# Performance work log

Measured on AMD Instinct MI355X. Metric: run time of the kernel, lower is better.

Reference implementation:

```python
import jax, jax.numpy as jnp
import numpy as np

NUM_NODES = 50000
NUM_HYPEREDGES = 50000
NNZ = 800000
IN_CH, HID_CH, OUT_CH = 512, 256, 64


def setup_inputs() -> dict:
    key = jax.random.key(0)
    k = jax.random.split(key, 6)
    x = jax.random.normal(k[0], (NUM_NODES, IN_CH), dtype=jnp.float32)
    node_idx = jax.random.randint(k[1], (NNZ,), 0, NUM_NODES)
    hedge_idx = jax.random.randint(k[2], (NNZ,), 0, NUM_HYPEREDGES)
    edge_index = jnp.stack([node_idx, hedge_idx]).astype(jnp.int64)
    W1 = jax.random.normal(k[3], (IN_CH, HID_CH), dtype=jnp.float32) * (1.0 / np.sqrt(IN_CH))
    b1 = jnp.zeros((HID_CH,), dtype=jnp.float32)
    W2 = jax.random.normal(k[4], (HID_CH, OUT_CH), dtype=jnp.float32) * (1.0 / np.sqrt(HID_CH))
    b2 = jnp.zeros((OUT_CH,), dtype=jnp.float32)
    return {"x": x, "edge_index": edge_index, "W1": W1, "b1": b1, "W2": W2, "b2": b2}


def hypergraph_conv(x, node_idx, hedge_idx, W, b):
    # x' = D^{-1} H B^{-1} H^T (x Theta) + b   (PyG HypergraphConv, unit edge weights)
    h = x @ W                                   # [N, F_out]
    ones = jnp.ones(node_idx.shape[0], dtype=x.dtype)
    D = jax.ops.segment_sum(ones, node_idx, num_segments=NUM_NODES)        # node degree
    B = jax.ops.segment_sum(ones, hedge_idx, num_segments=NUM_HYPEREDGES)  # hyperedge degree
    D_inv = jnp.where(D > 0, 1.0 / D, 0.0)
    B_inv = jnp.where(B > 0, 1.0 / B, 0.0)
    # node -> hyperedge aggregation
    m = jax.ops.segment_sum(h[node_idx], hedge_idx, num_segments=NUM_HYPEREDGES)
    m = m * B_inv[:, None]                      # [E, F_out]
    # hyperedge -> node aggregation
    out = jax.ops.segment_sum(m[hedge_idx], node_idx, num_segments=NUM_NODES)
    out = out * D_inv[:, None]                  # [N, F_out]
    return out + b


def reference(x, edge_index, W1, b1, W2, b2):
    node_idx = edge_index[0]
    hedge_idx = edge_index[1]
    h = hypergraph_conv(x, node_idx, hedge_idx, W1, b1)
    h = jax.nn.relu(h)
    h = hypergraph_conv(h, node_idx, hedge_idx, W2, b2)
    return jax.nn.log_softmax(h, axis=1)
```

## Files before the change

kernel.cpp:

```cpp
#include <hip/hip_runtime.h>
#include <math.h>

#define N_NODES  50000
#define N_HEDGES 50000
#define NNZ_     800000
#define IN_CH    512
#define HID_CH   256
#define OUT_CH   64
#define M_PAD    50048
#define NBK      391

#define BH_BLK   98
#define PK1_BLK  512
#define PK2_BLK  64

typedef __attribute__((ext_vector_type(8))) short bf16x8;
typedef __attribute__((ext_vector_type(4))) float f32x4;

__device__ __forceinline__ unsigned short f2bf(float f) {
    union { float f; unsigned u; } v; v.f = f;
    unsigned r = v.u + 0x7FFFu + ((v.u >> 16) & 1u);
    return (unsigned short)(r >> 16);
}
__device__ __forceinline__ float bf2f(unsigned short u) {
    union { unsigned u; float f; } v; v.u = (unsigned)u << 16; return v.f;
}

#define GLL16(g, l)                                                            \
    __builtin_amdgcn_global_load_lds(                                          \
        (const __attribute__((address_space(1))) void*)(g),                    \
        (__attribute__((address_space(3))) void*)(l), 16, 0, 0)

__global__ void prep_kernel(const float* __restrict__ W1, unsigned short* __restrict__ Wp1,
                            const float* __restrict__ W2, unsigned short* __restrict__ Wp2,
                            const int* __restrict__ ni, const int* __restrict__ hi,
                            int* __restrict__ bcntN, int* __restrict__ bcntH) {
    const int blk = blockIdx.x;
    const int t = threadIdx.x;
    if (blk < BH_BLK) {
        __shared__ int lh[NBK], ln[NBK];
        for (int k = t; k < NBK; k += 256) { lh[k] = 0; ln[k] = 0; }
        __syncthreads();
        for (int i4 = blk * 256 + t; i4 < NNZ_ / 4; i4 += BH_BLK * 256) {
            const int4 nv = *(const int4*)(ni + i4 * 4);
            const int4 hv = *(const int4*)(hi + i4 * 4);
            atomicAdd(&ln[nv.x >> 7], 1); atomicAdd(&ln[nv.y >> 7], 1);
            atomicAdd(&ln[nv.z >> 7], 1); atomicAdd(&ln[nv.w >> 7], 1);
            atomicAdd(&lh[hv.x >> 7], 1); atomicAdd(&lh[hv.y >> 7], 1);
            atomicAdd(&lh[hv.z >> 7], 1); atomicAdd(&lh[hv.w >> 7], 1);
        }
        __syncthreads();
        for (int k = t; k < NBK; k += 256) {
            if (ln[k]) atomicAdd(&bcntN[k], ln[k]);
            if (lh[k]) atomicAdd(&bcntH[k], lh[k]);
        }
    } else if (blk < BH_BLK + PK1_BLK) {
        const int i = (blk - BH_BLK) * 256 + t;
        const int kt = i / (HID_CH * 32);
        const int r  = i % (HID_CH * 32);
        const int n  = r >> 5, kk = r & 31;
        Wp1[i] = f2bf(W1[(size_t)(kt * 32 + kk) * HID_CH + n]);
    } else {
        const int i = (blk - (BH_BLK + PK1_BLK)) * 256 + t;
        const int kt = i / (OUT_CH * 32);
        const int r  = i % (OUT_CH * 32);
        const int n  = r >> 5, kk = r & 31;
        Wp2[i] = f2bf(W2[(size_t)(kt * 32 + kk) * OUT_CH + n]);
    }
}

__global__ void scan391_kernel(const int* __restrict__ cA, int* __restrict__ offA,
                               int* __restrict__ curA,
                               const int* __restrict__ cB, int* __restrict__ offB,
                               int* __restrict__ curB) {
    const int* cnt = blockIdx.x ? cB : cA;
    int* off = blockIdx.x ? offB : offA;
    int* cur = blockIdx.x ? curB : curA;
    __shared__ int sbuf[512];
    const int t = threadIdx.x;
    const int v = (t < NBK) ? cnt[t] : 0;
    sbuf[t] = v;
    __syncthreads();
    #pragma unroll
    for (int d = 1; d < 512; d <<= 1) {
        int u = (t >= d) ? sbuf[t - d] : 0;
        __syncthreads();
        sbuf[t] += u;
        __syncthreads();
    }
    if (t < NBK) { off[t] = sbuf[t] - v; cur[t] = sbuf[t] - v; }
    if (t == NBK - 1) off[NBK] = sbuf[t];
}

__global__ void bin_kernel(const int* __restrict__ ni, const int* __restrict__ hi,
                           int* __restrict__ bcurN, int* __restrict__ bcurH,
                           unsigned* __restrict__ recN, unsigned* __restrict__ recH) {
    __shared__ int cH[NBK], cN[NBK], bH[NBK], bN[NBK];
    for (int t = threadIdx.x; t < NBK; t += blockDim.x) { cH[t] = 0; cN[t] = 0; }
    __syncthreads();
    const int gid = blockIdx.x * blockDim.x + threadIdx.x;
    const int i0 = gid * 4;
    int4 nv, hv;
    const bool act = (i0 < NNZ_);
    if (act) {
        nv = *(const int4*)(ni + i0);
        hv = *(const int4*)(hi + i0);
        atomicAdd(&cN[nv.x >> 7], 1); atomicAdd(&cN[nv.y >> 7], 1);
        atomicAdd(&cN[nv.z >> 7], 1); atomicAdd(&cN[nv.w >> 7], 1);
        atomicAdd(&cH[hv.x >> 7], 1); atomicAdd(&cH[hv.y >> 7], 1);
        atomicAdd(&cH[hv.z >> 7], 1); atomicAdd(&cH[hv.w >> 7], 1);
    }
    __syncthreads();
    for (int t = threadIdx.x; t < NBK; t += blockDim.x) {
        bH[t] = cH[t] ? atomicAdd(&bcurH[t], cH[t]) : 0;
        bN[t] = cN[t] ? atomicAdd(&bcurN[t], cN[t]) : 0;
    }
    __syncthreads();
    for (int t = threadIdx.x; t < NBK; t += blockDim.x) { cH[t] = bH[t]; cN[t] = bN[t]; }
    __syncthreads();
    if (act) {
        int nn[4] = {nv.x, nv.y, nv.z, nv.w};
        int hh[4] = {hv.x, hv.y, hv.z, hv.w};
        #pragma unroll
        for (int k = 0; k < 4; ++k) {
            int p = atomicAdd(&cH[hh[k] >> 7], 1);
            recH[p] = ((unsigned)(hh[k] & 127) << 16) | (unsigned)nn[k];
            p = atomicAdd(&cN[nn[k] >> 7], 1);
            recN[p] = ((unsigned)(nn[k] & 127) << 16) | (unsigned)hh[k];
        }
    }
}

__global__ void buildcsr_kernel(const int* __restrict__ bstartH, const unsigned* __restrict__ recH,
                                int* __restrict__ offH, int* __restrict__ colH,
                                float* __restrict__ Binv,
                                const int* __restrict__ bstartN, const unsigned* __restrict__ recN,
                                int* __restrict__ offN, int* __restrict__ colN,
                                float* __restrict__ Dinv) {
    int b = blockIdx.x;
    const int* bstart; const unsigned* rec; int* off; int* col; float* inv;
    if (b < NBK) { bstart = bstartH; rec = recH; off = offH; col = colH; inv = Binv; }
    else { b -= NBK; bstart = bstartN; rec = recN; off = offN; col = colN; inv = Dinv; }
    const int s = bstart[b], e = bstart[b + 1];
    const int t = threadIdx.x;
    __shared__ int lc[128], ps[128], cur[128];
    if (t < 128) lc[t] = 0;
    __syncthreads();
    for (int i = s + t; i < e; i += 256) atomicAdd(&lc[rec[i] >> 16], 1);
    __syncthreads();
    if (t < 128) ps[t] = lc[t];
    __syncthreads();
    #pragma unroll
    for (int d = 1; d < 128; d <<= 1) {
        int v = (t >= d && t < 128) ? ps[t - d] : 0;
        __syncthreads();
        if (t < 128) ps[t] += v;
        __syncthreads();
    }
    if (t < 128) {
        const int excl = s + ps[t] - lc[t];
        cur[t] = excl;
        const int id = b * 128 + t;
        if (id < N_NODES) {
            off[id] = excl;
            inv[id] = lc[t] > 0 ? 1.f / (float)lc[t] : 0.f;
        }
    }
    if (b == NBK - 1 && t == 255) off[N_NODES] = bstart[NBK];
    __syncthreads();
    for (int i = s + t; i < e; i += 256) {
        const unsigned r = rec[i];
        const int p = atomicAdd(&cur[r >> 16], 1);
        col[p] = (int)(r & 0xFFFFu);
    }
}

__global__ void gemm1_fused_kernel(const float* __restrict__ X,
                                   const unsigned short* __restrict__ Wp,
                                   unsigned short* __restrict__ C, int M) {
    constexpr int BM = 64, BN = 256, K = IN_CH, KT = K / 32;
    __shared__ unsigned short As[BM * 32];
    __shared__ unsigned short Bs[BN * 32];
    const int tid  = threadIdx.x;
    const int wave = tid >> 6;
    const int lane = tid & 63;
    const int wr = wave >> 1;
    const int wc = wave & 1;
    const int quad = lane >> 4;
    const int l15  = lane & 15;
    const int row0 = blockIdx.x * BM;

    float4 va[2];
    auto loadA = [&](int kt) {
        #pragma unroll
        for (int r = 0; r < 2; ++r) {
            const int idx = r * 256 + tid;
            const int row = idx >> 3;
            const int kc  = (idx & 7) * 4;
            const int gr  = row0 + row;
            float4 v = make_float4(0.f, 0.f, 0.f, 0.f);
            if (gr < M) v = *(const float4*)(X + (size_t)gr * K + kt * 32 + kc);
            va[r] = v;
        }
    };

    f32x4 acc[2][8];
    #pragma unroll
    for (int mt = 0; mt < 2; ++mt)
        #pragma unroll
        for (int nt = 0; nt < 8; ++nt)
            acc[mt][nt] = (f32x4)0.f;

    loadA(0);
    for (int kt = 0; kt < KT; ++kt) {
        __syncthreads();
        #pragma unroll
        for (int r = 0; r < 2; ++r) {
            const int idx = r * 256 + tid;
            const int row = idx >> 3;
            const int kc  = (idx & 7) * 4;
            ushort4 o;
            o.x = f2bf(va[r].x); o.y = f2bf(va[r].y);
            o.z = f2bf(va[r].z); o.w = f2bf(va[r].w);
            *(ushort4*)(As + row * 32 + kc) = o;
        }
        const size_t bk = (size_t)kt * BN * 32;
        #pragma unroll
        for (int r = 0; r < 4; ++r)
            GLL16(Wp + bk + r * 2048 + (size_t)tid * 8, Bs + r * 2048 + tid * 8);
        __syncthreads();
        if (kt + 1 < KT) loadA(kt + 1);

        bf16x8 af[2], bfr[8];
        #pragma unroll
        for (int mt = 0; mt < 2; ++mt)
            af[mt] = *(const bf16x8*)(As + (wr * 32 + mt * 16 + l15) * 32 + quad * 8);
        #pragma unroll
        for (int nt = 0; nt < 8; ++nt)
            bfr[nt] = *(const bf16x8*)(Bs + (wc * 128 + nt * 16 + l15) * 32 + quad * 8);
        #pragma unroll
        for (int mt = 0; mt < 2; ++mt)
            #pragma unroll
            for (int nt = 0; nt < 8; ++nt)
                acc[mt][nt] = __builtin_amdgcn_mfma_f32_16x16x32_bf16(
                    af[mt], bfr[nt], acc[mt][nt], 0, 0, 0);
    }

    #pragma unroll
    for (int mt = 0; mt < 2; ++mt) {
        const int gr0 = row0 + wr * 32 + mt * 16 + quad * 4;
        #pragma unroll
        for (int nt = 0; nt < 8; ++nt) {
            const int gc = wc * 128 + nt * 16 + l15;
            #pragma unroll
            for (int r = 0; r < 4; ++r) {
                const int gr = gr0 + r;
                if (gr < M) C[(size_t)gr * HID_CH + gc] = f2bf(acc[mt][nt][r]);
            }
        }
    }
}

template <int BN>
__global__ void mfma_gemm_kernel(const unsigned short* __restrict__ A,
                                 const unsigned short* __restrict__ Wp,
                                 unsigned short* __restrict__ C, int M, int N, int K) {
    constexpr int NT = BN / 32;
    __shared__ unsigned short As[128 * 32];
    __shared__ unsigned short Bs[BN * 32];

    const int tid  = threadIdx.x;
    const int wave = tid >> 6;
    const int lane = tid & 63;
    const int wr = wave >> 1;
    const int wc = wave & 1;
    const int quad = lane >> 4;
    const int l15  = lane & 15;
    const int row0 = blockIdx.y * 128;
    const int col0 = blockIdx.x * BN;

    const size_t a_g0   = (size_t)(row0 + wave * 16 + (lane >> 2)) * K + (lane & 3) * 8;
    const int    a_l0   = (wave * 16 + (lane >> 2)) * 32 + (lane & 3) * 8;
    const size_t b_gbase = ((size_t)col0 + wave * 16 + (lane >> 2)) * 32 + (lane & 3) * 8;
    const int    b_l0   = (wave * 16 + (lane >> 2)) * 32 + (lane & 3) * 8;

    f32x4 acc[4][NT];
    #pragma unroll
    for (int mt = 0; mt < 4; ++mt)
        #pragma unroll
        for (int nt = 0; nt < NT; ++nt)
            acc[mt][nt] = (f32x4)0.f;

    const int KT = K / 32;
    for (int kt = 0; kt < KT; ++kt) {
        __syncthreads();
        GLL16(A + a_g0 + (size_t)kt * 32, As + a_l0);
        GLL16(A + a_g0 + (size_t)(kt * 32) + (size_t)64 * K, As + a_l0 + 64 * 32);
        const size_t bk = (size_t)kt * N * 32;
        GLL16(Wp + bk + b_gbase, Bs + b_l0);
        if (BN == 128)
            GLL16(Wp + bk + b_gbase + 64 * 32, Bs + b_l0 + 64 * 32);
        __syncthreads();

        bf16x8 af[4], bf[NT];
        #pragma unroll
        for (int mt = 0; mt < 4; ++mt)
            af[mt] = *(const bf16x8*)(As + (wr * 64 + mt * 16 + l15) * 32 + quad * 8);
        #pragma unroll
        for (int nt = 0; nt < NT; ++nt)
            bf[nt] = *(const bf16x8*)(Bs + (wc * (BN / 2) + nt * 16 + l15) * 32 + quad * 8);
        #pragma unroll
        for (int mt = 0; mt < 4; ++mt)
            #pragma unroll
            for (int nt = 0; nt < NT; ++nt)
                acc[mt][nt] = __builtin_amdgcn_mfma_f32_16x16x32_bf16(
                    af[mt], bf[nt], acc[mt][nt], 0, 0, 0);
    }

    #pragma unroll
    for (int mt = 0; mt < 4; ++mt) {
        const int gr0 = row0 + wr * 64 + mt * 16 + quad * 4;
        #pragma unroll
        for (int nt = 0; nt < NT; ++nt) {
            const int gc = col0 + wc * (BN / 2) + nt * 16 + l15;
            #pragma unroll
            for (int r = 0; r < 4; ++r) {
                int gr = gr0 + r;
                if (gr < M) C[(size_t)gr * N + gc] = f2bf(acc[mt][nt][r]);
            }
        }
    }
}

template <bool EPI>
__global__ void gather256_kernel(const unsigned short* __restrict__ src,
                                 unsigned short* __restrict__ dst,
                                 const int* __restrict__ off, const int* __restrict__ col,
                                 const float* __restrict__ scale,
                                 const float* __restrict__ bias, int nrows) {
    int row = blockIdx.x * (blockDim.x >> 6) + (threadIdx.x >> 6);
    if (row >= nrows) return;
    const int lane = threadIdx.x & 63;
    const int g = lane >> 5;
    const int l = lane & 31;
    const int s = off[row], e = off[row + 1];
    float a[8];
    #pragma unroll
    for (int k = 0; k < 8; ++k) a[k] = 0.f;
    int j = s + g;
    for (; j + 2 < e; j += 4) {
        const bf16x8 u0 = *(const bf16x8*)(src + ((size_t)col[j]     << 8) + (l << 3));
        const bf16x8 u1 = *(const bf16x8*)(src + ((size_t)col[j + 2] << 8) + (l << 3));
        #pragma unroll
        for (int k = 0; k < 8; ++k)
            a[k] += bf2f((unsigned short)u0[k]) + bf2f((unsigned short)u1[k]);
    }
    if (j < e) {
        const bf16x8 u = *(const bf16x8*)(src + ((size_t)col[j] << 8) + (l << 3));
        #pragma unroll
        for (int k = 0; k < 8; ++k) a[k] += bf2f((unsigned short)u[k]);
    }
    #pragma unroll
    for (int k = 0; k < 8; ++k) a[k] += __shfl_xor(a[k], 32);
    if (g != 0) return;
    const float sc = scale[row];
    float v[8];
    #pragma unroll
    for (int k = 0; k < 8; ++k) v[k] = a[k] * sc;
    if (EPI) {
        const float4 b0 = *(const float4*)(bias + (l << 3));
        const float4 b1 = *(const float4*)(bias + (l << 3) + 4);
        v[0] = fmaxf(v[0] + b0.x, 0.f); v[1] = fmaxf(v[1] + b0.y, 0.f);
        v[2] = fmaxf(v[2] + b0.z, 0.f); v[3] = fmaxf(v[3] + b0.w, 0.f);
        v[4] = fmaxf(v[4] + b1.x, 0.f); v[5] = fmaxf(v[5] + b1.y, 0.f);
        v[6] = fmaxf(v[6] + b1.z, 0.f); v[7] = fmaxf(v[7] + b1.w, 0.f);
    }
    bf16x8 o;
    #pragma unroll
    for (int k = 0; k < 8; ++k) o[k] = (short)f2bf(v[k]);
    *(bf16x8*)(dst + ((size_t)row << 8) + (l << 3)) = o;
}

template <bool LSM>
__global__ void gather64_kernel(const unsigned short* __restrict__ src, void* __restrict__ dstv,
                                const int* __restrict__ off, const int* __restrict__ col,
                                const float* __restrict__ scale,
                                const float* __restrict__ bias, int nrows) {
    int row = blockIdx.x * (blockDim.x >> 6) + (threadIdx.x >> 6);
    if (row >= nrows) return;
    const int lane = threadIdx.x & 63;
    const int g = lane >> 4;
    const int l = lane & 15;
    const int s = off[row], e = off[row + 1];
    float a0 = 0.f, a1 = 0.f, a2 = 0.f, a3 = 0.f;
    int j = s + g;
    for (; j + 4 < e; j += 8) {
        const ushort4 u0 = *(const ushort4*)(src + ((size_t)col[j]     << 6) + (l << 2));
        const ushort4 u1 = *(const ushort4*)(src + ((size_t)col[j + 4] << 6) + (l << 2));
        a0 += bf2f(u0.x) + bf2f(u1.x); a1 += bf2f(u0.y) + bf2f(u1.y);
        a2 += bf2f(u0.z) + bf2f(u1.z); a3 += bf2f(u0.w) + bf2f(u1.w);
    }
    if (j < e) {
        const ushort4 u = *(const ushort4*)(src + ((size_t)col[j] << 6) + (l << 2));
        a0 += bf2f(u.x); a1 += bf2f(u.y); a2 += bf2f(u.z); a3 += bf2f(u.w);
    }
    a0 += __shfl_xor(a0, 16); a1 += __shfl_xor(a1, 16);
    a2 += __shfl_xor(a2, 16); a3 += __shfl_xor(a3, 16);
    a0 += __shfl_xor(a0, 32); a1 += __shfl_xor(a1, 32);
    a2 += __shfl_xor(a2, 32); a3 += __shfl_xor(a3, 32);
    const float sc = scale[row];
    float v0 = a0 * sc, v1 = a1 * sc, v2 = a2 * sc, v3 = a3 * sc;
    if (LSM) {
        const float4 b = *(const float4*)(bias + (l << 2));
        v0 += b.x; v1 += b.y; v2 += b.z; v3 += b.w;
        float m = fmaxf(fmaxf(v0, v1), fmaxf(v2, v3));
        #pragma unroll
        for (int o = 8; o >= 1; o >>= 1) m = fmaxf(m, __shfl_xor(m, o));
        float su = expf(v0 - m) + expf(v1 - m) + expf(v2 - m) + expf(v3 - m);
        #pragma unroll
        for (int o = 8; o >= 1; o >>= 1) su += __shfl_xor(su, o);
        const float lg = m + logf(su);
        if (g == 0) {
            float4 o4;
            o4.x = v0 - lg; o4.y = v1 - lg; o4.z = v2 - lg; o4.w = v3 - lg;
            *(float4*)((float*)dstv + (size_t)row * OUT_CH + (l << 2)) = o4;
        }
    } else if (g == 0) {
        ushort4 o4;
        o4.x = f2bf(v0); o4.y = f2bf(v1); o4.z = f2bf(v2); o4.w = f2bf(v3);
        *(ushort4*)((unsigned short*)dstv + (size_t)row * OUT_CH + (l << 2)) = o4;
    }
}

extern "C" void kernel_launch(void* const* d_in, const int* in_sizes, int n_in,
                              void* d_out, int out_size, void* d_ws, size_t ws_size,
                              hipStream_t stream) {
    const float* x  = (const float*)d_in[0];
    const int*   ei = (const int*)d_in[1];
    const float* W1 = (const float*)d_in[2];
    const float* b1 = (const float*)d_in[3];
    const float* W2 = (const float*)d_in[4];
    const float* b2 = (const float*)d_in[5];
    float* out = (float*)d_out;

    const int* node_idx  = ei;
    const int* hedge_idx = ei + NNZ_;

    const size_t RCAP = (size_t)M_PAD * IN_CH / 2;
    float* regionA = (float*)d_ws;
    float* regionB = regionA + RCAP;
    float* Dinv = regionB + RCAP;
    float* Binv = Dinv + N_NODES;
    int* offN = (int*)(Binv + N_HEDGES);
    int* offH = offN + N_NODES + 1;
    int* colN = offH + N_HEDGES + 1;
    int* colH = colN + NNZ_;
    unsigned short* Wp1 = (unsigned short*)(colH + NNZ_);
    unsigned short* Wp2 = Wp1 + IN_CH * HID_CH;
    int* bcntH   = (int*)(Wp2 + HID_CH * OUT_CH);
    int* bcntN   = bcntH + 400;
    int* bstartH = bcntN + 400;
    int* bstartN = bstartH + 400;
    int* bcurH   = bstartN + 400;
    int* bcurN   = bcurH + 400;

    unsigned* recH = (unsigned*)regionA;
    unsigned* recN = recH + NNZ_;

    unsigned short* h1_bf = (unsigned short*)regionA;
    unsigned short* m1_bf = (unsigned short*)regionB;
    unsigned short* h2_bf = (unsigned short*)regionA;
    unsigned short* g_bf  = (unsigned short*)regionB;
    unsigned short* m2_bf = (unsigned short*)regionB + (size_t)M_PAD * OUT_CH;

    hipMemsetAsync(bcntH, 0, 800 * sizeof(int), stream);
    prep_kernel<<<BH_BLK + PK1_BLK + PK2_BLK, 256, 0, stream>>>(
        W1, Wp1, W2, Wp2, node_idx, hedge_idx, bcntN, bcntH);
    scan391_kernel<<<2, 512, 0, stream>>>(bcntH, bstartH, bcurH, bcntN, bstartN, bcurN);
    bin_kernel<<<200, 1024, 0, stream>>>(node_idx, hedge_idx, bcurN, bcurH, recN, recH);
    buildcsr_kernel<<<2 * NBK, 256, 0, stream>>>(bstartH, recH, offH, colH, Binv,
                                                 bstartN, recN, offN, colN, Dinv);

    gemm1_fused_kernel<<<(N_NODES + 63) / 64, 256, 0, stream>>>(x, Wp1, h1_bf, N_NODES);
    gather256_kernel<false><<<(N_HEDGES + 3) / 4, 256, 0, stream>>>(
        h1_bf, m1_bf, offH, colH, Binv, nullptr, N_HEDGES);
    gather256_kernel<true><<<(N_NODES + 3) / 4, 256, 0, stream>>>(
        m1_bf, h2_bf, offN, colN, Dinv, b1, N_NODES);

    mfma_gemm_kernel<64><<<dim3(OUT_CH / 64, (N_NODES + 127) / 128), 256, 0, stream>>>(
        h2_bf, Wp2, g_bf, N_NODES, OUT_CH, HID_CH);
    gather64_kernel<false><<<(N_HEDGES + 3) / 4, 256, 0, stream>>>(
        g_bf, m2_bf, offH, colH, Binv, nullptr, N_HEDGES);
    gather64_kernel<true><<<(N_NODES + 3) / 4, 256, 0, stream>>>(
        m2_bf, out, offN, colN, Dinv, b2, N_NODES);
}
```

Before: 401.8 us.

## Fuse CSR construction into one cooperative kernel and widen gather64 loads

Replaces the memset plus four preprocessing kernels (count, scan, bin, build CSR) with a single cooperative kernel that uses grid.sync between phases, cutting launch overhead and inter-kernel gaps. The bucket offsets are recomputed per block in shared memory instead of being stored to global memory. Separately, gather64 now has each lane load 8 bf16 values (16 bytes) instead of 4, with 8 neighbour groups per row, and the shuffle reductions are adjusted to match. The cooperative launch relies on 256 blocks of 1024 threads all being resident at once, and grid syncs add their own cost.

```diff
diff --git a/kernel.cpp b/kernel.cpp
--- a/kernel.cpp
+++ b/kernel.cpp
@@ -1,5 +1,8 @@
 #include <hip/hip_runtime.h>
+#include <hip/hip_cooperative_groups.h>
 #include <math.h>
+
+namespace cg = cooperative_groups;
 
 #define N_NODES  50000
 #define N_HEDGES 50000
@@ -10,10 +13,6 @@
 #define M_PAD    50048
 #define NBK      391
 
-#define BH_BLK   98
-#define PK1_BLK  512
-#define PK2_BLK  64
-
 typedef __attribute__((ext_vector_type(8))) short bf16x8;
 typedef __attribute__((ext_vector_type(4))) float f32x4;
 
@@ -31,147 +30,162 @@
         (const __attribute__((address_space(1))) void*)(g),                    \
         (__attribute__((address_space(3))) void*)(l), 16, 0, 0)
 
-__global__ void prep_kernel(const float* __restrict__ W1, unsigned short* __restrict__ Wp1,
-                            const float* __restrict__ W2, unsigned short* __restrict__ Wp2,
-                            const int* __restrict__ ni, const int* __restrict__ hi,
-                            int* __restrict__ bcntN, int* __restrict__ bcntH) {
+#define AST(p, v) __hip_atomic_store((p), (v), __ATOMIC_RELAXED, __HIP_MEMORY_SCOPE_AGENT)
+#define ALD(p)    __hip_atomic_load((p), __ATOMIC_RELAXED, __HIP_MEMORY_SCOPE_AGENT)
+
+__global__ __launch_bounds__(1024, 4) void csr_coop_kernel(
+    const float* __restrict__ W1, unsigned short* __restrict__ Wp1,
+    const float* __restrict__ W2, unsigned short* __restrict__ Wp2,
+    const int* __restrict__ ni, const int* __restrict__ hi,
+    int* __restrict__ cnts,
+    unsigned* __restrict__ recH, unsigned* __restrict__ recN,
+    int* __restrict__ offHg, int* __restrict__ colH, float* __restrict__ Binv,
+    int* __restrict__ offNg, int* __restrict__ colN, float* __restrict__ Dinv) {
+    cg::grid_group grid = cg::this_grid();
+    const int t = threadIdx.x;
     const int blk = blockIdx.x;
-    const int t = threadIdx.x;
-    if (blk < BH_BLK) {
-        __shared__ int lh[NBK], ln[NBK];
-        for (int k = t; k < NBK; k += 256) { lh[k] = 0; ln[k] = 0; }
-        __syncthreads();
-        for (int i4 = blk * 256 + t; i4 < NNZ_ / 4; i4 += BH_BLK * 256) {
-            const int4 nv = *(const int4*)(ni + i4 * 4);
-            const int4 hv = *(const int4*)(hi + i4 * 4);
-            atomicAdd(&ln[nv.x >> 7], 1); atomicAdd(&ln[nv.y >> 7], 1);
-            atomicAdd(&ln[nv.z >> 7], 1); atomicAdd(&ln[nv.w >> 7], 1);
-            atomicAdd(&lh[hv.x >> 7], 1); atomicAdd(&lh[hv.y >> 7], 1);
-            atomicAdd(&lh[hv.z >> 7], 1); atomicAdd(&lh[hv.w >> 7], 1);
-        }
-        __syncthreads();
-        for (int k = t; k < NBK; k += 256) {
-            if (ln[k]) atomicAdd(&bcntN[k], ln[k]);
-            if (lh[k]) atomicAdd(&bcntH[k], lh[k]);
-        }
-    } else if (blk < BH_BLK + PK1_BLK) {
-        const int i = (blk - BH_BLK) * 256 + t;
-        const int kt = i / (HID_CH * 32);
-        const int r  = i % (HID_CH * 32);
-        const int n  = r >> 5, kk = r & 31;
-        Wp1[i] = f2bf(W1[(size_t)(kt * 32 + kk) * HID_CH + n]);
-    } else {
-        const int i = (blk - (BH_BLK + PK1_BLK)) * 256 + t;
-        const int kt = i / (OUT_CH * 32);
-        const int r  = i % (OUT_CH * 32);
-        const int n  = r >> 5, kk = r & 31;
-        Wp2[i] = f2bf(W2[(size_t)(kt * 32 + kk) * OUT_CH + n]);
-    }
-}
-
-__global__ void scan391_kernel(const int* __restrict__ cA, int* __restrict__ offA,
-                               int* __restrict__ curA,
-                               const int* __restrict__ cB, int* __restrict__ offB,
-                               int* __restrict__ curB) {
-    const int* cnt = blockIdx.x ? cB : cA;
-    int* off = blockIdx.x ? offB : offA;
-    int* cur = blockIdx.x ? curB : curA;
-    __shared__ int sbuf[512];
-    const int t = threadIdx.x;
-    const int v = (t < NBK) ? cnt[t] : 0;
-    sbuf[t] = v;
+    const int gtid = blk * 1024 + t;
+
+    __shared__ int offH[NBK + 1], offN[NBK + 1];
+    __shared__ int sA[512], sB[512];
+    __shared__ int cH[NBK], cN[NBK], bH[NBK], bN[NBK];
+    __shared__ int lc[128], ps[128], cur[128];
+
+    if (blk == 0) {
+        for (int i = t; i < 1600; i += 1024) AST(&cnts[i], 0);
+    }
+    grid.sync();
+
+    for (int k = t; k < NBK; k += 1024) { cH[k] = 0; cN[k] = 0; }
     __syncthreads();
-    #pragma unroll
-    for (int d = 1; d < 512; d <<= 1) {
-        int u = (t >= d) ? sbuf[t - d] : 0;
-        __syncthreads();
-        sbuf[t] += u;
-        __syncthreads();
-    }
-    if (t < NBK) { off[t] = sbuf[t] - v; cur[t] = sbuf[t] - v; }
-    if (t == NBK - 1) off[NBK] = sbuf[t];
-}
-
-__global__ void bin_kernel(const int* __restrict__ ni, const int* __restrict__ hi,
-                           int* __restrict__ bcurN, int* __restrict__ bcurH,
-                           unsigned* __restrict__ recN, unsigned* __restrict__ recH) {
-    __shared__ int cH[NBK], cN[NBK], bH[NBK], bN[NBK];
-    for (int t = threadIdx.x; t < NBK; t += blockDim.x) { cH[t] = 0; cN[t] = 0; }
-    __syncthreads();
-    const int gid = blockIdx.x * blockDim.x + threadIdx.x;
-    const int i0 = gid * 4;
-    int4 nv, hv;
-    const bool act = (i0 < NNZ_);
-    if (act) {
-        nv = *(const int4*)(ni + i0);
-        hv = *(const int4*)(hi + i0);
+    if (gtid < NNZ_ / 4) {
+        const int4 nv = *(const int4*)(ni + gtid * 4);
+        const int4 hv = *(const int4*)(hi + gtid * 4);
         atomicAdd(&cN[nv.x >> 7], 1); atomicAdd(&cN[nv.y >> 7], 1);
         atomicAdd(&cN[nv.z >> 7], 1); atomicAdd(&cN[nv.w >> 7], 1);
         atomicAdd(&cH[hv.x >> 7], 1); atomicAdd(&cH[hv.y >> 7], 1);
         atomicAdd(&cH[hv.z >> 7], 1); atomicAdd(&cH[hv.w >> 7], 1);
     }
+    if (gtid < IN_CH * HID_CH) {
+        const int kt = gtid / (HID_CH * 32);
+        const int r  = gtid % (HID_CH * 32);
+        const int n  = r >> 5, kk = r & 31;
+        Wp1[gtid] = f2bf(W1[(size_t)(kt * 32 + kk) * HID_CH + n]);
+    }
+    if (gtid < HID_CH * OUT_CH) {
+        const int kt = gtid / (OUT_CH * 32);
+        const int r  = gtid % (OUT_CH * 32);
+        const int n  = r >> 5, kk = r & 31;
+        Wp2[gtid] = f2bf(W2[(size_t)(kt * 32 + kk) * OUT_CH + n]);
+    }
     __syncthreads();
-    for (int t = threadIdx.x; t < NBK; t += blockDim.x) {
-        bH[t] = cH[t] ? atomicAdd(&bcurH[t], cH[t]) : 0;
-        bN[t] = cN[t] ? atomicAdd(&bcurN[t], cN[t]) : 0;
-    }
+    for (int k = t; k < NBK; k += 1024) {
+        if (cH[k]) atomicAdd(&cnts[k], cH[k]);
+        if (cN[k]) atomicAdd(&cnts[400 + k], cN[k]);
+    }
+    grid.sync();
+
+    {
+        int vH = 0, vN = 0;
+        if (t < 512) {
+            vH = (t < NBK) ? ALD(&cnts[t]) : 0;
+            sA[t] = vH;
+        } else {
+            const int tt = t - 512;
+            vN = (tt < NBK) ? ALD(&cnts[400 + tt]) : 0;
+            sB[tt] = vN;
+        }
+        __syncthreads();
+        #pragma unroll
+        for (int d = 1; d < 512; d <<= 1) {
+            int u = 0;
+            if (t < 512) { if (t >= d) u = sA[t - d]; }
+            else { const int tt = t - 512; if (tt >= d) u = sB[tt - d]; }
+            __syncthreads();
+            if (t < 512) sA[t] += u; else sB[t - 512] += u;
+            __syncthreads();
+        }
+        if (t < NBK) offH[t] = sA[t] - vH;
+        if (t >= 512 && t - 512 < NBK) offN[t - 512] = sB[t - 512] - vN;
+        if (t == NBK - 1) offH[NBK] = sA[t];
+        if (t - 512 == NBK - 1) offN[NBK] = sB[t - 512];
+        __syncthreads();
+    }
+
+    for (int k = t; k < NBK; k += 1024) { cH[k] = 0; cN[k] = 0; }
     __syncthreads();
-    for (int t = threadIdx.x; t < NBK; t += blockDim.x) { cH[t] = bH[t]; cN[t] = bN[t]; }
+    const int i0 = gtid * 4;
+    const bool act = (i0 < NNZ_);
+    int4 nv4, hv4;
+    if (act) {
+        nv4 = *(const int4*)(ni + i0);
+        hv4 = *(const int4*)(hi + i0);
+        atomicAdd(&cN[nv4.x >> 7], 1); atomicAdd(&cN[nv4.y >> 7], 1);
+        atomicAdd(&cN[nv4.z >> 7], 1); atomicAdd(&cN[nv4.w >> 7], 1);
+        atomicAdd(&cH[hv4.x >> 7], 1); atomicAdd(&cH[hv4.y >> 7], 1);
+        atomicAdd(&cH[hv4.z >> 7], 1); atomicAdd(&cH[hv4.w >> 7], 1);
+    }
+    __syncthreads();
+    for (int k = t; k < NBK; k += 1024) {
+        bH[k] = cH[k] ? offH[k] + atomicAdd(&cnts[800 + k], cH[k]) : 0;
+        bN[k] = cN[k] ? offN[k] + atomicAdd(&cnts[1200 + k], cN[k]) : 0;
+    }
+    __syncthreads();
+    for (int k = t; k < NBK; k += 1024) { cH[k] = bH[k]; cN[k] = bN[k]; }
     __syncthreads();
     if (act) {
-        int nn[4] = {nv.x, nv.y, nv.z, nv.w};
-        int hh[4] = {hv.x, hv.y, hv.z, hv.w};
+        const int nn[4] = {nv4.x, nv4.y, nv4.z, nv4.w};
+        const int hh[4] = {hv4.x, hv4.y, hv4.z, hv4.w};
         #pragma unroll
         for (int k = 0; k < 4; ++k) {
             int p = atomicAdd(&cH[hh[k] >> 7], 1);
-            recH[p] = ((unsigned)(hh[k] & 127) << 16) | (unsigned)nn[k];
+            AST(&recH[p], ((unsigned)(hh[k] & 127) << 16) | (unsigned)nn[k]);
             p = atomicAdd(&cN[nn[k] >> 7], 1);
-            recN[p] = ((unsigned)(nn[k] & 127) << 16) | (unsigned)hh[k];
-        }
-    }
-}
-
-__global__ void buildcsr_kernel(const int* __restrict__ bstartH, const unsigned* __restrict__ recH,
-                                int* __restrict__ offH, int* __restrict__ colH,
-                                float* __restrict__ Binv,
-                                const int* __restrict__ bstartN, const unsigned* __restrict__ recN,
-                                int* __restrict__ offN, int* __restrict__ colN,
-                                float* __restrict__ Dinv) {
-    int b = blockIdx.x;
-    const int* bstart; const unsigned* rec; int* off; int* col; float* inv;
-    if (b < NBK) { bstart = bstartH; rec = recH; off = offH; col = colH; inv = Binv; }
-    else { b -= NBK; bstart = bstartN; rec = recN; off = offN; col = colN; inv = Dinv; }
-    const int s = bstart[b], e = bstart[b + 1];
-    const int t = threadIdx.x;
-    __shared__ int lc[128], ps[128], cur[128];
-    if (t < 128) lc[t] = 0;
-    __syncthreads();
-    for (int i = s + t; i < e; i += 256) atomicAdd(&lc[rec[i] >> 16], 1);
-    __syncthreads();
-    if (t < 128) ps[t] = lc[t];
-    __syncthreads();
-    #pragma unroll
-    for (int d = 1; d < 128; d <<= 1) {
-        int v = (t >= d && t < 128) ? ps[t - d] : 0;
-        __syncthreads();
-        if (t < 128) ps[t] += v;
-        __syncthreads();
-    }
-    if (t < 128) {
-        const int excl = s + ps[t] - lc[t];
-        cur[t] = excl;
-        const int id = b * 128 + t;
-        if (id < N_NODES) {
-            off[id] = excl;
-            inv[id] = lc[t] > 0 ? 1.f / (float)lc[t] : 0.f;
-        }
-    }
-    if (b == NBK - 1 && t == 255) off[N_NODES] = bstart[NBK];
-    __syncthreads();
-    for (int i = s + t; i < e; i += 256) {
-        const unsigned r = rec[i];
-        const int p = atomicAdd(&cur[r >> 16], 1);
-        col[p] = (int)(r & 0xFFFFu);
+            AST(&recN[p], ((unsigned)(nn[k] & 127) << 16) | (unsigned)hh[k]);
+        }
+    }
+    grid.sync();
+
+    for (int vb = blk; vb < 2 * NBK; vb += gridDim.x) {
+        const bool isH = vb < NBK;
+        const int b = isH ? vb : vb - NBK;
+        const int s = isH ? offH[b] : offN[b];
+        const int e = isH ? offH[b + 1] : offN[b + 1];
+        const unsigned* rec = isH ? recH : recN;
+        int* off = isH ? offHg : offNg;
+        int* col = isH ? colH : colN;
+        float* inv = isH ? Binv : Dinv;
+        __syncthreads();
+        if (t < 128) lc[t] = 0;
+        __syncthreads();
+        for (int i = s + t; i < e; i += 1024)
+            atomicAdd(&lc[(int)(ALD(&rec[i]) >> 16)], 1);
+        __syncthreads();
+        if (t < 128) ps[t] = lc[t];
+        __syncthreads();
+        #pragma unroll
+        for (int d = 1; d < 128; d <<= 1) {
+            const int v = (t < 128 && t >= d) ? ps[t - d] : 0;
+            __syncthreads();
+            if (t < 128) ps[t] += v;
+            __syncthreads();
+        }
+        if (t < 128) {
+            const int excl = s + ps[t] - lc[t];
+            cur[t] = excl;
+            const int id = b * 128 + t;
+            if (id < N_NODES) {
+                off[id] = excl;
+                inv[id] = lc[t] > 0 ? 1.f / (float)lc[t] : 0.f;
+            }
+        }
+        if (b == NBK - 1 && t == 0) off[N_NODES] = isH ? offH[NBK] : offN[NBK];
+        __syncthreads();
+        for (int i = s + t; i < e; i += 1024) {
+            const unsigned r = ALD(&rec[i]);
+            const int p = atomicAdd(&cur[r >> 16], 1);
+            col[p] = (int)(r & 0xFFFFu);
+        }
     }
 }
 
@@ -389,46 +403,66 @@
     int row = blockIdx.x * (blockDim.x >> 6) + (threadIdx.x >> 6);
     if (row >= nrows) return;
     const int lane = threadIdx.x & 63;
-    const int g = lane >> 4;
-    const int l = lane & 15;
+    const int g = lane >> 3;
+    const int l = lane & 7;
     const int s = off[row], e = off[row + 1];
-    float a0 = 0.f, a1 = 0.f, a2 = 0.f, a3 = 0.f;
+    float a[8];
+    #pragma unroll
+    for (int k = 0; k < 8; ++k) a[k] = 0.f;
     int j = s + g;
-    for (; j + 4 < e; j += 8) {
-        const ushort4 u0 = *(const ushort4*)(src + ((size_t)col[j]     << 6) + (l << 2));
-        const ushort4 u1 = *(const ushort4*)(src + ((size_t)col[j + 4] << 6) + (l << 2));
-        a0 += bf2f(u0.x) + bf2f(u1.x); a1 += bf2f(u0.y) + bf2f(u1.y);
-        a2 += bf2f(u0.z) + bf2f(u1.z); a3 += bf2f(u0.w) + bf2f(u1.w);
+    for (; j + 8 < e; j += 16) {
+        const bf16x8 u0 = *(const bf16x8*)(src + ((size_t)col[j]     << 6) + (l << 3));
+        const bf16x8 u1 = *(const bf16x8*)(src + ((size_t)col[j + 8] << 6) + (l << 3));
+        #pragma unroll
+        for (int k = 0; k < 8; ++k)
+            a[k] += bf2f((unsigned short)u0[k]) + bf2f((unsigned short)u1[k]);
     }
     if (j < e) {
-        const ushort4 u = *(const ushort4*)(src + ((size_t)col[j] << 6) + (l << 2));
-        a0 += bf2f(u.x); a1 += bf2f(u.y); a2 += bf2f(u.z); a3 += bf2f(u.w);
-    }
-    a0 += __shfl_xor(a0, 16); a1 += __shfl_xor(a1, 16);
-    a2 += __shfl_xor(a2, 16); a3 += __shfl_xor(a3, 16);
-    a0 += __shfl_xor(a0, 32); a1 += __shfl_xor(a1, 32);
-    a2 += __shfl_xor(a2, 32); a3 += __shfl_xor(a3, 32);
+        const bf16x8 u = *(const bf16x8*)(src + ((size_t)col[j] << 6) + (l << 3));
+        #pragma unroll
+        for (int k = 0; k < 8; ++k) a[k] += bf2f((unsigned short)u[k]);
+    }
+    #pragma unroll
+    for (int k = 0; k < 8; ++k) {
+        a[k] += __shfl_xor(a[k], 8);
+        a[k] += __shfl_xor(a[k], 16);
+        a[k] += __shfl_xor(a[k], 32);
+    }
     const float sc = scale[row];
-    float v0 = a0 * sc, v1 = a1 * sc, v2 = a2 * sc, v3 = a3 * sc;
+    float v[8];
+    #pragma unroll
+    for (int k = 0; k < 8; ++k) v[k] = a[k] * sc;
     if (LSM) {
-        const float4 b = *(const float4*)(bias + (l << 2));
-        v0 += b.x; v1 += b.y; v2 += b.z; v3 += b.w;
-        float m = fmaxf(fmaxf(v0, v1), fmaxf(v2, v3));
-        #pragma unroll
-        for (int o = 8; o >= 1; o >>= 1) m = fmaxf(m, __shfl_xor(m, o));
-        float su = expf(v0 - m) + expf(v1 - m) + expf(v2 - m) + expf(v3 - m);
-        #pragma unroll
-        for (int o = 8; o >= 1; o >>= 1) su += __shfl_xor(su, o);
+        const float4 b0 = *(const float4*)(bias + (l << 3));
+        const float4 b1 = *(const float4*)(bias + (l << 3) + 4);
+        v[0] += b0.x; v[1] += b0.y; v[2] += b0.z; v[3] += b0.w;
+        v[4] += b1.x; v[5] += b1.y; v[6] += b1.z; v[7] += b1.w;
+        float m = v[0];
+        #pragma unroll
+        for (int k = 1; k < 8; ++k) m = fmaxf(m, v[k]);
+        m = fmaxf(m, __shfl_xor(m, 1));
+        m = fmaxf(m, __shfl_xor(m, 2));
+        m = fmaxf(m, __shfl_xor(m, 4));
+        float su = 0.f;
+        #pragma unroll
+        for (int k = 0; k < 8; ++k) su += expf(v[k] - m);
+        su += __shfl_xor(su, 1);
+        su += __shfl_xor(su, 2);
+        su += __shfl_xor(su, 4);
         const float lg = m + logf(su);
         if (g == 0) {
-            float4 o4;
-            o4.x = v0 - lg; o4.y = v1 - lg; o4.z = v2 - lg; o4.w = v3 - lg;
-            *(float4*)((float*)dstv + (size_t)row * OUT_CH + (l << 2)) = o4;
+            float* dp = (float*)dstv + (size_t)row * OUT_CH + (l << 3);
+            float4 o0, o1;
+            o0.x = v[0] - lg; o0.y = v[1] - lg; o0.z = v[2] - lg; o0.w = v[3] - lg;
+            o1.x = v[4] - lg; o1.y = v[5] - lg; o1.z = v[6] - lg; o1.w = v[7] - lg;
+            *(float4*)dp = o0;
+            *(float4*)(dp + 4) = o1;
         }
     } else if (g == 0) {
-        ushort4 o4;
-        o4.x = f2bf(v0); o4.y = f2bf(v1); o4.z = f2bf(v2); o4.w = f2bf(v3);
-        *(ushort4*)((unsigned short*)dstv + (size_t)row * OUT_CH + (l << 2)) = o4;
+        bf16x8 o;
+        #pragma unroll
+        for (int k = 0; k < 8; ++k) o[k] = (short)f2bf(v[k]);
+        *(bf16x8*)((unsigned short*)dstv + (size_t)row * OUT_CH + (l << 3)) = o;
     }
 }
 
@@ -457,12 +491,7 @@
     int* colH = colN + NNZ_;
     unsigned short* Wp1 = (unsigned short*)(colH + NNZ_);
     unsigned short* Wp2 = Wp1 + IN_CH * HID_CH;
-    int* bcntH   = (int*)(Wp2 + HID_CH * OUT_CH);
-    int* bcntN   = bcntH + 400;
-    int* bstartH = bcntN + 400;
-    int* bstartN = bstartH + 400;
-    int* bcurH   = bstartN + 400;
-    int* bcurN   = bcurH + 400;
+    int* cnts = (int*)(Wp2 + HID_CH * OUT_CH);
 
     unsigned* recH = (unsigned*)regionA;
     unsigned* recN = recH + NNZ_;
@@ -473,13 +502,19 @@
     unsigned short* g_bf  = (unsigned short*)regionB;
     unsigned short* m2_bf = (unsigned short*)regionB + (size_t)M_PAD * OUT_CH;
 
-    hipMemsetAsync(bcntH, 0, 800 * sizeof(int), stream);
-    prep_kernel<<<BH_BLK + PK1_BLK + PK2_BLK, 256, 0, stream>>>(
-        W1, Wp1, W2, Wp2, node_idx, hedge_idx, bcntN, bcntH);
-    scan391_kernel<<<2, 512, 0, stream>>>(bcntH, bstartH, bcurH, bcntN, bstartN, bcurN);
-    bin_kernel<<<200, 1024, 0, stream>>>(node_idx, hedge_idx, bcurN, bcurH, recN, recH);
-    buildcsr_kernel<<<2 * NBK, 256, 0, stream>>>(bstartH, recH, offH, colH, Binv,
-                                                 bstartN, recN, offN, colN, Dinv);
+    {
+        const float* a0 = W1; unsigned short* a1 = Wp1;
+        const float* a2 = W2; unsigned short* a3 = Wp2;
+        const int* a4 = node_idx; const int* a5 = hedge_idx;
+        int* a6 = cnts;
+        unsigned* a7 = recH; unsigned* a8 = recN;
+        int* a9 = offH; int* a10 = colH; float* a11 = Binv;
+        int* a12 = offN; int* a13 = colN; float* a14 = Dinv;
+        void* args[] = {&a0, &a1, &a2, &a3, &a4, &a5, &a6, &a7,
+                        &a8, &a9, &a10, &a11, &a12, &a13, &a14};
+        hipLaunchCooperativeKernel((void*)csr_coop_kernel, dim3(256), dim3(1024),
+                                   args, 0, stream);
+    }
 
     gemm1_fused_kernel<<<(N_NODES + 63) / 64, 256, 0, stream>>>(x, Wp1, h1_bf, N_NODES);
     gather256_kernel<false><<<(N_HEDGES + 3) / 4, 256, 0, stream>>>(
```

Result: slower. 489.7 us (+21.9%).
